# Kernel tuning notes

Hardware: AMD Instinct MI355X
Metric: run time of the kernel (lower is better)

The kernel has to match this reference:

```python
import jax, jax.numpy as jnp
from jax import lax
import numpy as np

B, S, D, H, O = 16384, 128, 512, 1024, 10


def setup_inputs() -> dict:
    key = jax.random.key(0)
    ks = jax.random.split(key, 7)
    def lin(kw, kb, out_d, in_d):
        bound = 1.0 / np.sqrt(in_d)
        w = jax.random.uniform(kw, (out_d, in_d), jnp.float32, -bound, bound)
        b = jax.random.uniform(kb, (out_d,), jnp.float32, -bound, bound)
        return w, b
    x = jax.random.normal(ks[0], (B, D), jnp.float32)
    Whx_w, Whx_b = lin(ks[1], ks[2], H, D)
    Whh_w, Whh_b = lin(ks[3], ks[4], H, H)
    Wph_w, Wph_b = lin(ks[5], ks[6], O, H)
    return {"x": x, "Whx_w": Whx_w, "Whx_b": Whx_b, "Whh_w": Whh_w,
            "Whh_b": Whh_b, "Wph_w": Wph_w, "Wph_b": Wph_b, "seq_length": S}


def reference(x, Whx_w, Whx_b, Whh_w, Whh_b, Wph_w, Wph_b, seq_length):
    # The original forward feeds the SAME x at every timestep, so the
    # input projection W_hx(x) is a loop-invariant we compute once.
    xW = x @ Whx_w.T + Whx_b  # [B, H]

    def step(h, _):
        h = jnp.tanh(xW + h @ Whh_w.T + Whh_b)
        return h, None

    h0 = jnp.zeros((x.shape[0], Whh_w.shape[0]), x.dtype)  # h starts at 0
    h, _ = lax.scan(step, h0, None, length=seq_length)
    out = h @ Wph_w.T + Wph_b  # [B, O]
    return jax.nn.softmax(out, axis=-1)
```

## Files before the change

kernel.cpp:

```cpp
#include <hip/hip_runtime.h>

#define BATCH    16384
#define H_DIM    1024
#define D_DIM    512
#define O_DIM    10
#define SEQ      128
#define BM       64
#define NTHREADS 1024
#define HSTR     1040
#define HBUF_SZ  (BM * HSTR)
#define QW       (127.0f / 0.03125f)
#define QSCALE   (0.03125f / (127.0f * 127.0f))

typedef __bf16 bf16;
typedef __bf16 bf16x8 __attribute__((ext_vector_type(8)));
typedef float  f32x16 __attribute__((ext_vector_type(16)));
typedef float  f32x4  __attribute__((ext_vector_type(4)));
typedef int    i32x4  __attribute__((ext_vector_type(4)));
typedef int    i32x16 __attribute__((ext_vector_type(16)));

__device__ bf16        g_x[BATCH * D_DIM];
__device__ bf16        g_whx[H_DIM * D_DIM];
__device__ signed char g_whhq[H_DIM * H_DIM];
__device__ bf16        g_wph[O_DIM * H_DIM];
__device__ bf16        g_xwp[BATCH * H_DIM];
__device__ float       g_bias[H_DIM];
__device__ float       g_bph[O_DIM];

__device__ __forceinline__ float fast_tanh(float z) {
  float e = __expf(2.0f * z);
  return 1.0f - 2.0f / (e + 1.0f);
}

__global__ void cvt_bf16(const float* __restrict__ src, bf16* __restrict__ dst, int n) {
  const int i = (blockIdx.x * blockDim.x + threadIdx.x) * 8;
  if (i >= n) return;
  f32x4 s0 = *(const f32x4*)(src + i);
  f32x4 s1 = *(const f32x4*)(src + i + 4);
  bf16x8 v;
  #pragma unroll
  for (int j = 0; j < 4; ++j) { v[j] = (bf16)s0[j]; v[4 + j] = (bf16)s1[j]; }
  *(bf16x8*)(dst + i) = v;
}

__global__ void pack_whhq(const float* __restrict__ src, signed char* __restrict__ dst) {
  const int t = blockIdx.x * blockDim.x + threadIdx.x;
  const int lane = t & 63;
  const int nt   = (t >> 6) & 1;
  const int kc   = (t >> 7) & 31;
  const int w    = t >> 12;
  const int row = w * 64 + nt * 32 + (lane & 31);
  const int col = kc * 32 + (lane >> 5) * 16;
  const float* s = src + (size_t)row * H_DIM + col;
  #pragma unroll
  for (int j = 0; j < 16; ++j) {
    int q = (int)lrintf(s[j] * QW);
    q = q > 127 ? 127 : (q < -127 ? -127 : q);
    dst[(size_t)t * 16 + j] = (signed char)q;
  }
}

__global__ void cvt_bias(const float* __restrict__ bx, const float* __restrict__ bh,
                         const float* __restrict__ bp) {
  const int i = blockIdx.x * blockDim.x + threadIdx.x;
  if (i < H_DIM) g_bias[i] = bx[i] + bh[i];
  if (i < O_DIM) g_bph[i]  = bp[i];
}

#define MFMA4_BF16(A0, A1, B)                                                            \
  accf[0][0] = __builtin_amdgcn_mfma_f32_32x32x16_bf16(A0, (B)[0], accf[0][0], 0, 0, 0); \
  accf[0][1] = __builtin_amdgcn_mfma_f32_32x32x16_bf16(A0, (B)[1], accf[0][1], 0, 0, 0); \
  accf[1][0] = __builtin_amdgcn_mfma_f32_32x32x16_bf16(A1, (B)[0], accf[1][0], 0, 0, 0); \
  accf[1][1] = __builtin_amdgcn_mfma_f32_32x32x16_bf16(A1, (B)[1], accf[1][1], 0, 0, 0);

#define MFMA4_I8(A0, A1, B)                                                              \
  acc[0][0] = __builtin_amdgcn_mfma_i32_32x32x32_i8(A0, (B)[0], acc[0][0], 0, 0, 0);     \
  acc[0][1] = __builtin_amdgcn_mfma_i32_32x32x32_i8(A0, (B)[1], acc[0][1], 0, 0, 0);     \
  acc[1][0] = __builtin_amdgcn_mfma_i32_32x32x32_i8(A1, (B)[0], acc[1][0], 0, 0, 0);     \
  acc[1][1] = __builtin_amdgcn_mfma_i32_32x32x32_i8(A1, (B)[1], acc[1][1], 0, 0, 0);

#define LDS_BARRIER()                                      \
  asm volatile("s_waitcnt lgkmcnt(0)" ::: "memory");       \
  __builtin_amdgcn_s_barrier();                            \
  asm volatile("" ::: "memory");

__global__ __launch_bounds__(NTHREADS, 3)
void rnn_fused(float* __restrict__ out)
{
  extern __shared__ char smem[];
  signed char* hcur = (signed char*)smem;
  signed char* hnxt = (signed char*)smem + HBUF_SZ;

  const int tid  = threadIdx.x;
  const int wave = tid >> 6;
  const int lane = tid & 63;
  const int m31  = lane & 31;
  const int q    = lane >> 5;
  const int r0   = blockIdx.x * BM;
  const int nw0  = wave * 64;

  const signed char* bstr = g_whhq + (size_t)wave * (32 * 2 * 1024) + lane * 16;
  bf16* xbase = g_xwp + ((size_t)blockIdx.x * 16 + wave) * 4096 + lane * 8;

  i32x4 bq[4][2];

  {
    f32x16 accf[2][2];
    #pragma unroll
    for (int mt = 0; mt < 2; ++mt)
      #pragma unroll
      for (int nt = 0; nt < 2; ++nt)
        #pragma unroll
        for (int i = 0; i < 16; ++i) accf[mt][nt][i] = 0.0f;

    const bf16* aBase = g_x + (size_t)(r0 + m31) * D_DIM + q * 8;
    #pragma unroll 4
    for (int kc = 0; kc < D_DIM / 16; ++kc) {
      bf16x8 a0 = *(const bf16x8*)(aBase + kc * 16);
      bf16x8 a1 = *(const bf16x8*)(aBase + (size_t)32 * D_DIM + kc * 16);
      bf16x8 b[2];
      #pragma unroll
      for (int nt = 0; nt < 2; ++nt)
        b[nt] = *(const bf16x8*)(g_whx + (size_t)(nw0 + nt * 32 + m31) * D_DIM + kc * 16 + q * 8);
      MFMA4_BF16(a0, a1, b);
    }

    bf16x8 xq[8];
    #pragma unroll
    for (int nt = 0; nt < 2; ++nt) {
      const int col = nw0 + nt * 32 + m31;
      const float bias = g_bias[col];
      #pragma unroll
      for (int mt = 0; mt < 2; ++mt)
        #pragma unroll
        for (int r = 0; r < 16; ++r) {
          const int row = mt * 32 + (r & 3) + 8 * (r >> 2) + 4 * q;
          const int idx = (nt * 2 + mt) * 16 + r;
          const float v = accf[mt][nt][r] + bias;
          xq[idx >> 3][idx & 7] = (bf16)v;
          hcur[row * HSTR + col] = (signed char)__float2int_rn(fast_tanh(v) * 127.0f);
        }
    }
    #pragma unroll
    for (int i = 0; i < 8; ++i)
      __builtin_nontemporal_store(xq[i], (bf16x8*)(xbase + i * 512));
  }

  asm volatile("s_waitcnt vmcnt(0)" ::: "memory");

  #pragma unroll
  for (int p = 0; p < 4; ++p)
    #pragma unroll
    for (int nt = 0; nt < 2; ++nt)
      bq[p][nt] = *(const i32x4*)(bstr + (p * 2 + nt) * 1024);

  LDS_BARRIER()

  const int aoff = m31 * HSTR + q * 16;

  for (int step = 1; step < SEQ; ++step) {
    i32x16 acc[2][2];
    #pragma unroll
    for (int mt = 0; mt < 2; ++mt)
      #pragma unroll
      for (int nt = 0; nt < 2; ++nt)
        #pragma unroll
        for (int i = 0; i < 16; ++i) acc[mt][nt][i] = 0;

    const signed char* aP0 = hcur + aoff;
    const signed char* aP1 = aP0 + 32 * HSTR;

    __builtin_amdgcn_s_setprio(1);
    #pragma unroll
    for (int kc = 0; kc < 32; ++kc) {
      i32x4 a0 = *(const i32x4*)(aP0 + kc * 32);
      i32x4 a1 = *(const i32x4*)(aP1 + kc * 32);
      MFMA4_I8(a0, a1, bq[kc & 3]);
      #pragma unroll
      for (int nt = 0; nt < 2; ++nt)
        bq[kc & 3][nt] = *(const i32x4*)(bstr + ((((kc + 4) & 31) * 2 + nt) * 1024));
    }
    __builtin_amdgcn_s_setprio(0);

    bf16x8 xq[8];
    #pragma unroll
    for (int i = 0; i < 8; ++i)
      xq[i] = __builtin_nontemporal_load((const bf16x8*)(xbase + i * 512));

    #pragma unroll
    for (int nt = 0; nt < 2; ++nt) {
      const int col = nw0 + nt * 32 + m31;
      #pragma unroll
      for (int mt = 0; mt < 2; ++mt)
        #pragma unroll
        for (int r = 0; r < 16; ++r) {
          const int row = mt * 32 + (r & 3) + 8 * (r >> 2) + 4 * q;
          const int idx = (nt * 2 + mt) * 16 + r;
          const float v = (float)acc[mt][nt][r] * QSCALE + (float)xq[idx >> 3][idx & 7];
          hnxt[row * HSTR + col] = (signed char)__float2int_rn(fast_tanh(v) * 127.0f);
        }
    }

    LDS_BARRIER()
    signed char* t = hcur; hcur = hnxt; hnxt = t;
  }

  {
    const int row  = tid >> 4;
    const int tsub = tid & 15;
    float p[O_DIM];
    #pragma unroll
    for (int o = 0; o < O_DIM; ++o) p[o] = 0.0f;

    const signed char* hrow = hcur + row * HSTR + tsub * 64;
    for (int kk = 0; kk < 64; kk += 16) {
      i32x4 hp = *(const i32x4*)(hrow + kk);
      float hf[16];
      #pragma unroll
      for (int d = 0; d < 4; ++d)
        #pragma unroll
        for (int j = 0; j < 4; ++j)
          hf[d * 4 + j] = (float)((int)(hp[d] << ((3 - j) * 8)) >> 24);
      #pragma unroll
      for (int o = 0; o < O_DIM; ++o) {
        bf16x8 wv0 = *(const bf16x8*)(g_wph + (size_t)o * H_DIM + tsub * 64 + kk);
        bf16x8 wv1 = *(const bf16x8*)(g_wph + (size_t)o * H_DIM + tsub * 64 + kk + 8);
        #pragma unroll
        for (int j = 0; j < 8; ++j) {
          p[o] += hf[j] * (float)wv0[j];
          p[o] += hf[8 + j] * (float)wv1[j];
        }
      }
    }
    #pragma unroll
    for (int d = 1; d < 16; d <<= 1)
      #pragma unroll
      for (int o = 0; o < O_DIM; ++o) p[o] += __shfl_xor(p[o], d, 16);

    if (tsub == 0) {
      float v[O_DIM], mx = -1e30f;
      #pragma unroll
      for (int o = 0; o < O_DIM; ++o) {
        v[o] = p[o] * (1.0f / 127.0f) + g_bph[o];
        mx = fmaxf(mx, v[o]);
      }
      float s = 0.0f;
      #pragma unroll
      for (int o = 0; o < O_DIM; ++o) { v[o] = __expf(v[o] - mx); s += v[o]; }
      const float inv = 1.0f / s;
      #pragma unroll
      for (int o = 0; o < O_DIM; ++o)
        out[(size_t)(r0 + row) * O_DIM + o] = v[o] * inv;
    }
  }
}

extern "C" void kernel_launch(void* const* d_in, const int* in_sizes, int n_in,
                              void* d_out, int out_size, void* d_ws, size_t ws_size,
                              hipStream_t stream)
{
  (void)d_ws; (void)ws_size; (void)in_sizes; (void)n_in; (void)out_size;
  const float* x     = (const float*)d_in[0];
  const float* Whx_w = (const float*)d_in[1];
  const float* Whx_b = (const float*)d_in[2];
  const float* Whh_w = (const float*)d_in[3];
  const float* Whh_b = (const float*)d_in[4];
  const float* Wph_w = (const float*)d_in[5];
  const float* Wph_b = (const float*)d_in[6];
  float* out = (float*)d_out;

  (void)hipFuncSetAttribute((const void*)rnn_fused,
                            hipFuncAttributeMaxDynamicSharedMemorySize, 2 * HBUF_SZ);

  bf16* gx; bf16* gwhx; signed char* gwhhq; bf16* gwph;
  hipGetSymbolAddress((void**)&gx,    HIP_SYMBOL(g_x));
  hipGetSymbolAddress((void**)&gwhx,  HIP_SYMBOL(g_whx));
  hipGetSymbolAddress((void**)&gwhhq, HIP_SYMBOL(g_whhq));
  hipGetSymbolAddress((void**)&gwph,  HIP_SYMBOL(g_wph));

  cvt_bf16<<<BATCH * D_DIM / 2048, 256, 0, stream>>>(x,     gx,   BATCH * D_DIM);
  cvt_bf16<<<H_DIM * D_DIM / 2048, 256, 0, stream>>>(Whx_w, gwhx, H_DIM * D_DIM);
  pack_whhq<<<65536 / 256, 256, 0, stream>>>(Whh_w, gwhhq);
  cvt_bf16<<<(O_DIM * H_DIM / 8 + 255) / 256, 256, 0, stream>>>(Wph_w, gwph, O_DIM * H_DIM);
  cvt_bias<<<4, 256, 0, stream>>>(Whx_b, Whh_b, Wph_b);

  const dim3 grid(BATCH / BM), block(NTHREADS);
  const size_t lds = 2 * HBUF_SZ;
  rnn_fused<<<grid, block, lds, stream>>>(out);
}
```

Before: 4.615 ms.

## Stage W_hh tiles through LDS via direct global-to-LDS loads, single h buffer

Replaces the register-held 4-deep prefetch of the int8 W_hh B-fragments with per-wave double-buffered staging in LDS using global_load_lds, paced by explicit vmcnt waits. The h double buffer is collapsed into a single LDS buffer, with an extra barrier before the write-back to protect readers. The xW preload is moved earlier into the K loop to overlap with the MFMAs. The aim is to free VGPRs and hide global-load latency. The cost is an extra barrier per step and more LDS traffic, and the hand-written vmcnt counting is fragile.

```diff
diff --git a/kernel.cpp b/kernel.cpp
--- a/kernel.cpp
+++ b/kernel.cpp
@@ -9,8 +9,13 @@
 #define NTHREADS 1024
 #define HSTR     1040
 #define HBUF_SZ  (BM * HSTR)
+#define BSTG_OFF HBUF_SZ
+#define LDS_TOT  (HBUF_SZ + 16 * 4096)
 #define QW       (127.0f / 0.03125f)
 #define QSCALE   (0.03125f / (127.0f * 127.0f))
+
+#define AS1 __attribute__((address_space(1)))
+#define AS3 __attribute__((address_space(3)))
 
 typedef __bf16 bf16;
 typedef __bf16 bf16x8 __attribute__((ext_vector_type(8)));
@@ -73,12 +78,6 @@
   accf[1][0] = __builtin_amdgcn_mfma_f32_32x32x16_bf16(A1, (B)[0], accf[1][0], 0, 0, 0); \
   accf[1][1] = __builtin_amdgcn_mfma_f32_32x32x16_bf16(A1, (B)[1], accf[1][1], 0, 0, 0);
 
-#define MFMA4_I8(A0, A1, B)                                                              \
-  acc[0][0] = __builtin_amdgcn_mfma_i32_32x32x32_i8(A0, (B)[0], acc[0][0], 0, 0, 0);     \
-  acc[0][1] = __builtin_amdgcn_mfma_i32_32x32x32_i8(A0, (B)[1], acc[0][1], 0, 0, 0);     \
-  acc[1][0] = __builtin_amdgcn_mfma_i32_32x32x32_i8(A1, (B)[0], acc[1][0], 0, 0, 0);     \
-  acc[1][1] = __builtin_amdgcn_mfma_i32_32x32x32_i8(A1, (B)[1], acc[1][1], 0, 0, 0);
-
 #define LDS_BARRIER()                                      \
   asm volatile("s_waitcnt lgkmcnt(0)" ::: "memory");       \
   __builtin_amdgcn_s_barrier();                            \
@@ -88,8 +87,7 @@
 void rnn_fused(float* __restrict__ out)
 {
   extern __shared__ char smem[];
-  signed char* hcur = (signed char*)smem;
-  signed char* hnxt = (signed char*)smem + HBUF_SZ;
+  signed char* hbuf = (signed char*)smem;
 
   const int tid  = threadIdx.x;
   const int wave = tid >> 6;
@@ -99,10 +97,16 @@
   const int r0   = blockIdx.x * BM;
   const int nw0  = wave * 64;
 
-  const signed char* bstr = g_whhq + (size_t)wave * (32 * 2 * 1024) + lane * 16;
+  const signed char* bsrc = g_whhq + (size_t)wave * 65536 + lane * 16;
+  char* myB  = smem + BSTG_OFF + wave * 4096;
+  const signed char* myBr = (const signed char*)myB + lane * 16;
   bf16* xbase = g_xwp + ((size_t)blockIdx.x * 16 + wave) * 4096 + lane * 8;
 
-  i32x4 bq[4][2];
+  #define STAGE(KT)                                                                        \
+    __builtin_amdgcn_global_load_lds((const AS1 void*)(bsrc + (KT) * 2048),                \
+                                     (AS3 void*)(myB + ((KT) & 1) * 2048), 16, 0, 0);      \
+    __builtin_amdgcn_global_load_lds((const AS1 void*)(bsrc + (KT) * 2048 + 1024),         \
+                                     (AS3 void*)(myB + ((KT) & 1) * 2048 + 1024), 16, 0, 0);
 
   {
     f32x16 accf[2][2];
@@ -125,7 +129,7 @@
       MFMA4_BF16(a0, a1, b);
     }
 
-    bf16x8 xq[8];
+    bf16x8 xq0[8];
     #pragma unroll
     for (int nt = 0; nt < 2; ++nt) {
       const int col = nw0 + nt * 32 + m31;
@@ -137,26 +141,24 @@
           const int row = mt * 32 + (r & 3) + 8 * (r >> 2) + 4 * q;
           const int idx = (nt * 2 + mt) * 16 + r;
           const float v = accf[mt][nt][r] + bias;
-          xq[idx >> 3][idx & 7] = (bf16)v;
-          hcur[row * HSTR + col] = (signed char)__float2int_rn(fast_tanh(v) * 127.0f);
+          xq0[idx >> 3][idx & 7] = (bf16)v;
+          hbuf[row * HSTR + col] = (signed char)__float2int_rn(fast_tanh(v) * 127.0f);
         }
     }
     #pragma unroll
     for (int i = 0; i < 8; ++i)
-      __builtin_nontemporal_store(xq[i], (bf16x8*)(xbase + i * 512));
+      __builtin_nontemporal_store(xq0[i], (bf16x8*)(xbase + i * 512));
   }
 
   asm volatile("s_waitcnt vmcnt(0)" ::: "memory");
 
-  #pragma unroll
-  for (int p = 0; p < 4; ++p)
-    #pragma unroll
-    for (int nt = 0; nt < 2; ++nt)
-      bq[p][nt] = *(const i32x4*)(bstr + (p * 2 + nt) * 1024);
+  STAGE(0)
+  STAGE(1)
 
   LDS_BARRIER()
 
-  const int aoff = m31 * HSTR + q * 16;
+  const signed char* aP0 = hbuf + m31 * HSTR + q * 16;
+  const signed char* aP1 = aP0 + 32 * HSTR;
 
   for (int step = 1; step < SEQ; ++step) {
     i32x16 acc[2][2];
@@ -167,25 +169,37 @@
         #pragma unroll
         for (int i = 0; i < 16; ++i) acc[mt][nt][i] = 0;
 
-    const signed char* aP0 = hcur + aoff;
-    const signed char* aP1 = aP0 + 32 * HSTR;
+    bf16x8 xq[8];
 
     __builtin_amdgcn_s_setprio(1);
     #pragma unroll
     for (int kc = 0; kc < 32; ++kc) {
+      if (kc < 30) { asm volatile("s_waitcnt vmcnt(2)" ::: "memory"); }
+      else         { asm volatile("s_waitcnt vmcnt(10)" ::: "memory"); }
+
+      i32x4 b0 = *(const i32x4*)(myBr + (kc & 1) * 2048);
+      i32x4 b1 = *(const i32x4*)(myBr + (kc & 1) * 2048 + 1024);
       i32x4 a0 = *(const i32x4*)(aP0 + kc * 32);
       i32x4 a1 = *(const i32x4*)(aP1 + kc * 32);
-      MFMA4_I8(a0, a1, bq[kc & 3]);
-      #pragma unroll
-      for (int nt = 0; nt < 2; ++nt)
-        bq[kc & 3][nt] = *(const i32x4*)(bstr + ((((kc + 4) & 31) * 2 + nt) * 1024));
+      acc[0][0] = __builtin_amdgcn_mfma_i32_32x32x32_i8(a0, b0, acc[0][0], 0, 0, 0);
+      acc[0][1] = __builtin_amdgcn_mfma_i32_32x32x32_i8(a0, b1, acc[0][1], 0, 0, 0);
+      acc[1][0] = __builtin_amdgcn_mfma_i32_32x32x32_i8(a1, b0, acc[1][0], 0, 0, 0);
+      acc[1][1] = __builtin_amdgcn_mfma_i32_32x32x32_i8(a1, b1, acc[1][1], 0, 0, 0);
+
+      __builtin_amdgcn_sched_barrier(0);
+      STAGE((kc + 2) & 31)
+
+      if (kc == 29) {
+        #pragma unroll
+        for (int i = 0; i < 8; ++i)
+          xq[i] = __builtin_nontemporal_load((const bf16x8*)(xbase + i * 512));
+      }
     }
     __builtin_amdgcn_s_setprio(0);
 
-    bf16x8 xq[8];
-    #pragma unroll
-    for (int i = 0; i < 8; ++i)
-      xq[i] = __builtin_nontemporal_load((const bf16x8*)(xbase + i * 512));
+    asm volatile("s_waitcnt vmcnt(4)" ::: "memory");
+
+    LDS_BARRIER()
 
     #pragma unroll
     for (int nt = 0; nt < 2; ++nt) {
@@ -197,12 +211,11 @@
           const int row = mt * 32 + (r & 3) + 8 * (r >> 2) + 4 * q;
           const int idx = (nt * 2 + mt) * 16 + r;
           const float v = (float)acc[mt][nt][r] * QSCALE + (float)xq[idx >> 3][idx & 7];
-          hnxt[row * HSTR + col] = (signed char)__float2int_rn(fast_tanh(v) * 127.0f);
+          hbuf[row * HSTR + col] = (signed char)__float2int_rn(fast_tanh(v) * 127.0f);
         }
     }
 
     LDS_BARRIER()
-    signed char* t = hcur; hcur = hnxt; hnxt = t;
   }
 
   {
@@ -212,7 +225,7 @@
     #pragma unroll
     for (int o = 0; o < O_DIM; ++o) p[o] = 0.0f;
 
-    const signed char* hrow = hcur + row * HSTR + tsub * 64;
+    const signed char* hrow = hbuf + row * HSTR + tsub * 64;
     for (int kk = 0; kk < 64; kk += 16) {
       i32x4 hp = *(const i32x4*)(hrow + kk);
       float hf[16];
@@ -270,7 +283,7 @@
   float* out = (float*)d_out;
 
   (void)hipFuncSetAttribute((const void*)rnn_fused,
-                            hipFuncAttributeMaxDynamicSharedMemorySize, 2 * HBUF_SZ);
+                            hipFuncAttributeMaxDynamicSharedMemorySize, LDS_TOT);
 
   bf16* gx; bf16* gwhx; signed char* gwhhq; bf16* gwph;
   hipGetSymbolAddress((void**)&gx,    HIP_SYMBOL(g_x));
@@ -285,6 +298,5 @@
   cvt_bias<<<4, 256, 0, stream>>>(Whx_b, Whh_b, Wph_b);
 
   const dim3 grid(BATCH / BM), block(NTHREADS);
-  const size_t lds = 2 * HBUF_SZ;
-  rnn_fused<<<grid, block, lds, stream>>>(out);
-}
+  rnn_fused<<<grid, block, LDS_TOT, stream>>>(out);
+}
```

Result: slower. 4.986 ms (+8.0%).

## Halve batch tile to 32 rows with 8 waves covering 128 columns each

Applied to the files above, without the earlier changes.

Shrinks the per-block batch tile from 64 to 32 rows and the block from 16 to 8 waves. Each wave now sweeps two 64-column panels per step, reloading its int8 W_hh fragments from global/L2 for each panel, and the packed weight layout is changed to match. This doubles the number of blocks and raises the occupancy target to 4 blocks per CU, which is meant to add parallelism and latency hiding. The cost is that every weight fragment is now reused across only 32 rows instead of 64, so W_hh traffic per row doubles, and the per-step global reads are more serialized.

```diff
diff --git a/kernel.cpp b/kernel.cpp
--- a/kernel.cpp
+++ b/kernel.cpp
@@ -5,8 +5,8 @@
 #define D_DIM    512
 #define O_DIM    10
 #define SEQ      128
-#define BM       64
-#define NTHREADS 1024
+#define BM       32
+#define NTHREADS 512
 #define HSTR     1040
 #define HBUF_SZ  (BM * HSTR)
 #define QW       (127.0f / 0.03125f)
@@ -48,8 +48,9 @@
   const int lane = t & 63;
   const int nt   = (t >> 6) & 1;
   const int kc   = (t >> 7) & 31;
-  const int w    = t >> 12;
-  const int row = w * 64 + nt * 32 + (lane & 31);
+  const int p    = (t >> 12) & 1;
+  const int w    = t >> 13;
+  const int row = w * 128 + p * 64 + nt * 32 + (lane & 31);
   const int col = kc * 32 + (lane >> 5) * 16;
   const float* s = src + (size_t)row * H_DIM + col;
   #pragma unroll
@@ -67,24 +68,12 @@
   if (i < O_DIM) g_bph[i]  = bp[i];
 }
 
-#define MFMA4_BF16(A0, A1, B)                                                            \
-  accf[0][0] = __builtin_amdgcn_mfma_f32_32x32x16_bf16(A0, (B)[0], accf[0][0], 0, 0, 0); \
-  accf[0][1] = __builtin_amdgcn_mfma_f32_32x32x16_bf16(A0, (B)[1], accf[0][1], 0, 0, 0); \
-  accf[1][0] = __builtin_amdgcn_mfma_f32_32x32x16_bf16(A1, (B)[0], accf[1][0], 0, 0, 0); \
-  accf[1][1] = __builtin_amdgcn_mfma_f32_32x32x16_bf16(A1, (B)[1], accf[1][1], 0, 0, 0);
-
-#define MFMA4_I8(A0, A1, B)                                                              \
-  acc[0][0] = __builtin_amdgcn_mfma_i32_32x32x32_i8(A0, (B)[0], acc[0][0], 0, 0, 0);     \
-  acc[0][1] = __builtin_amdgcn_mfma_i32_32x32x32_i8(A0, (B)[1], acc[0][1], 0, 0, 0);     \
-  acc[1][0] = __builtin_amdgcn_mfma_i32_32x32x32_i8(A1, (B)[0], acc[1][0], 0, 0, 0);     \
-  acc[1][1] = __builtin_amdgcn_mfma_i32_32x32x32_i8(A1, (B)[1], acc[1][1], 0, 0, 0);
-
 #define LDS_BARRIER()                                      \
   asm volatile("s_waitcnt lgkmcnt(0)" ::: "memory");       \
   __builtin_amdgcn_s_barrier();                            \
   asm volatile("" ::: "memory");
 
-__global__ __launch_bounds__(NTHREADS, 3)
+__global__ __launch_bounds__(NTHREADS, 4)
 void rnn_fused(float* __restrict__ out)
 {
   extern __shared__ char smem[];
@@ -97,108 +86,119 @@
   const int m31  = lane & 31;
   const int q    = lane >> 5;
   const int r0   = blockIdx.x * BM;
-  const int nw0  = wave * 64;
-
-  const signed char* bstr = g_whhq + (size_t)wave * (32 * 2 * 1024) + lane * 16;
-  bf16* xbase = g_xwp + ((size_t)blockIdx.x * 16 + wave) * 4096 + lane * 8;
-
-  i32x4 bq[4][2];
+  const int nw0  = wave * 128;
+
+  const signed char* bstr = g_whhq + (size_t)wave * 131072 + lane * 16;
+  bf16* xwbase = g_xwp + ((size_t)blockIdx.x * 8 + wave) * 4096 + lane * 8;
+
+  i32x4 bq[2][2];
 
   {
-    f32x16 accf[2][2];
-    #pragma unroll
-    for (int mt = 0; mt < 2; ++mt)
+    const bf16* aBase = g_x + (size_t)(r0 + m31) * D_DIM + q * 8;
+    #pragma unroll
+    for (int p = 0; p < 2; ++p) {
+      f32x16 accf[2];
       #pragma unroll
       for (int nt = 0; nt < 2; ++nt)
         #pragma unroll
-        for (int i = 0; i < 16; ++i) accf[mt][nt][i] = 0.0f;
-
-    const bf16* aBase = g_x + (size_t)(r0 + m31) * D_DIM + q * 8;
-    #pragma unroll 4
-    for (int kc = 0; kc < D_DIM / 16; ++kc) {
-      bf16x8 a0 = *(const bf16x8*)(aBase + kc * 16);
-      bf16x8 a1 = *(const bf16x8*)(aBase + (size_t)32 * D_DIM + kc * 16);
-      bf16x8 b[2];
+        for (int i = 0; i < 16; ++i) accf[nt][i] = 0.0f;
+
+      const int cb = nw0 + p * 64;
+      #pragma unroll 4
+      for (int kc = 0; kc < D_DIM / 16; ++kc) {
+        bf16x8 a0 = *(const bf16x8*)(aBase + kc * 16);
+        #pragma unroll
+        for (int nt = 0; nt < 2; ++nt) {
+          bf16x8 b = *(const bf16x8*)(g_whx + (size_t)(cb + nt * 32 + m31) * D_DIM + kc * 16 + q * 8);
+          accf[nt] = __builtin_amdgcn_mfma_f32_32x32x16_bf16(a0, b, accf[nt], 0, 0, 0);
+        }
+      }
+
+      bf16* xb = xwbase + p * 2048;
+      bf16x8 xs[4];
+      #pragma unroll
+      for (int nt = 0; nt < 2; ++nt) {
+        const int col = cb + nt * 32 + m31;
+        const float bias = g_bias[col];
+        #pragma unroll
+        for (int r = 0; r < 16; ++r) {
+          const int row = (r & 3) + 8 * (r >> 2) + 4 * q;
+          const int idx = nt * 16 + r;
+          const float v = accf[nt][r] + bias;
+          xs[idx >> 3][idx & 7] = (bf16)v;
+          hcur[row * HSTR + col] = (signed char)__float2int_rn(fast_tanh(v) * 127.0f);
+        }
+      }
+      #pragma unroll
+      for (int f = 0; f < 4; ++f)
+        __builtin_nontemporal_store(xs[f], (bf16x8*)(xb + f * 512));
+    }
+  }
+
+  asm volatile("s_waitcnt vmcnt(0)" ::: "memory");
+
+  #pragma unroll
+  for (int k = 0; k < 2; ++k)
+    #pragma unroll
+    for (int nt = 0; nt < 2; ++nt)
+      bq[k][nt] = *(const i32x4*)(bstr + k * 2048 + nt * 1024);
+
+  LDS_BARRIER()
+
+  const int aoff = m31 * HSTR + q * 16;
+
+  for (int step = 1; step < SEQ; ++step) {
+    const signed char* aP = hcur + aoff;
+
+    #pragma unroll
+    for (int p = 0; p < 2; ++p) {
+      const bf16* xb = xwbase + p * 2048;
+      bf16x8 xq[4];
+      #pragma unroll
+      for (int f = 0; f < 4; ++f)
+        xq[f] = __builtin_nontemporal_load((const bf16x8*)(xb + f * 512));
+
+      i32x16 acc[2];
       #pragma unroll
       for (int nt = 0; nt < 2; ++nt)
-        b[nt] = *(const bf16x8*)(g_whx + (size_t)(nw0 + nt * 32 + m31) * D_DIM + kc * 16 + q * 8);
-      MFMA4_BF16(a0, a1, b);
-    }
-
-    bf16x8 xq[8];
-    #pragma unroll
-    for (int nt = 0; nt < 2; ++nt) {
-      const int col = nw0 + nt * 32 + m31;
-      const float bias = g_bias[col];
-      #pragma unroll
-      for (int mt = 0; mt < 2; ++mt)
+        #pragma unroll
+        for (int i = 0; i < 16; ++i) acc[nt][i] = 0;
+
+      const signed char* bp = bstr + p * 65536;
+
+      __builtin_amdgcn_s_setprio(1);
+      #pragma unroll
+      for (int kc = 0; kc < 32; ++kc) {
+        i32x4 a0 = *(const i32x4*)(aP + kc * 32);
+        acc[0] = __builtin_amdgcn_mfma_i32_32x32x32_i8(a0, bq[kc & 1][0], acc[0], 0, 0, 0);
+        acc[1] = __builtin_amdgcn_mfma_i32_32x32x32_i8(a0, bq[kc & 1][1], acc[1], 0, 0, 0);
+        if (kc < 30) {
+          #pragma unroll
+          for (int nt = 0; nt < 2; ++nt)
+            bq[kc & 1][nt] = *(const i32x4*)(bp + (kc + 2) * 2048 + nt * 1024);
+        }
+      }
+      __builtin_amdgcn_s_setprio(0);
+
+      const signed char* bpn = bstr + (p ^ 1) * 65536;
+      #pragma unroll
+      for (int k = 0; k < 2; ++k)
+        #pragma unroll
+        for (int nt = 0; nt < 2; ++nt)
+          bq[k][nt] = *(const i32x4*)(bpn + k * 2048 + nt * 1024);
+
+      const int cb = nw0 + p * 64;
+      #pragma unroll
+      for (int nt = 0; nt < 2; ++nt) {
+        const int col = cb + nt * 32 + m31;
         #pragma unroll
         for (int r = 0; r < 16; ++r) {
-          const int row = mt * 32 + (r & 3) + 8 * (r >> 2) + 4 * q;
-          const int idx = (nt * 2 + mt) * 16 + r;
-          const float v = accf[mt][nt][r] + bias;
-          xq[idx >> 3][idx & 7] = (bf16)v;
-          hcur[row * HSTR + col] = (signed char)__float2int_rn(fast_tanh(v) * 127.0f);
-        }
-    }
-    #pragma unroll
-    for (int i = 0; i < 8; ++i)
-      __builtin_nontemporal_store(xq[i], (bf16x8*)(xbase + i * 512));
-  }
-
-  asm volatile("s_waitcnt vmcnt(0)" ::: "memory");
-
-  #pragma unroll
-  for (int p = 0; p < 4; ++p)
-    #pragma unroll
-    for (int nt = 0; nt < 2; ++nt)
-      bq[p][nt] = *(const i32x4*)(bstr + (p * 2 + nt) * 1024);
-
-  LDS_BARRIER()
-
-  const int aoff = m31 * HSTR + q * 16;
-
-  for (int step = 1; step < SEQ; ++step) {
-    i32x16 acc[2][2];
-    #pragma unroll
-    for (int mt = 0; mt < 2; ++mt)
-      #pragma unroll
-      for (int nt = 0; nt < 2; ++nt)
-        #pragma unroll
-        for (int i = 0; i < 16; ++i) acc[mt][nt][i] = 0;
-
-    const signed char* aP0 = hcur + aoff;
-    const signed char* aP1 = aP0 + 32 * HSTR;
-
-    __builtin_amdgcn_s_setprio(1);
-    #pragma unroll
-    for (int kc = 0; kc < 32; ++kc) {
-      i32x4 a0 = *(const i32x4*)(aP0 + kc * 32);
-      i32x4 a1 = *(const i32x4*)(aP1 + kc * 32);
-      MFMA4_I8(a0, a1, bq[kc & 3]);
-      #pragma unroll
-      for (int nt = 0; nt < 2; ++nt)
-        bq[kc & 3][nt] = *(const i32x4*)(bstr + ((((kc + 4) & 31) * 2 + nt) * 1024));
-    }
-    __builtin_amdgcn_s_setprio(0);
-
-    bf16x8 xq[8];
-    #pragma unroll
-    for (int i = 0; i < 8; ++i)
-      xq[i] = __builtin_nontemporal_load((const bf16x8*)(xbase + i * 512));
-
-    #pragma unroll
-    for (int nt = 0; nt < 2; ++nt) {
-      const int col = nw0 + nt * 32 + m31;
-      #pragma unroll
-      for (int mt = 0; mt < 2; ++mt)
-        #pragma unroll
-        for (int r = 0; r < 16; ++r) {
-          const int row = mt * 32 + (r & 3) + 8 * (r >> 2) + 4 * q;
-          const int idx = (nt * 2 + mt) * 16 + r;
-          const float v = (float)acc[mt][nt][r] * QSCALE + (float)xq[idx >> 3][idx & 7];
+          const int row = (r & 3) + 8 * (r >> 2) + 4 * q;
+          const int idx = nt * 16 + r;
+          const float v = (float)acc[nt][r] * QSCALE + (float)xq[idx >> 3][idx & 7];
           hnxt[row * HSTR + col] = (signed char)__float2int_rn(fast_tanh(v) * 127.0f);
         }
+      }
     }
 
     LDS_BARRIER()
```

Result: slower. 7.537 ms (+63.3%).
